# Optimization experiments

Hardware: AMD Instinct MI355X
Metric: run time of the kernel (lower is better)

The kernel has to match this reference:

```python
import jax, jax.numpy as jnp
import numpy as np

NUM_LEVELS = 6
LEVEL_DIM = 4
BASE_RES = 4
HASHMAP_SIZE = 2 ** 19  # torch-ngp default log2_hashmap_size=19
N_SAMPLES = 300
PRIMES = (1, 2654435761, 805459861)
N_RAYS = 16384

# offsets of the 8 trilinear corners, [8,3]
_OFFS = jnp.array([[i, j, k] for i in (0, 1) for j in (0, 1) for k in (0, 1)], dtype=jnp.int32)


def _sample_points_along_ray(starts, ends):
    # starts/ends: [N,2]; lerp 300 points, append ray parameter t as z -> [N,300,3]
    t = jnp.linspace(0.0, 1.0, N_SAMPLES, dtype=starts.dtype)[None, :, None]  # [1,300,1]
    p2 = starts[:, None, :] * (1.0 - t) + ends[:, None, :] * t  # [N,300,2]
    z = jnp.broadcast_to(t, (starts.shape[0], N_SAMPLES, 1))
    return jnp.concatenate([p2, z], axis=-1)


def _grid_encode(points, embeddings):
    # points: [N,S,3] in [0,1]; embeddings: [L, T, D]. Returns [N,S,L*D].
    feats = []
    for l in range(NUM_LEVELS):
        R = BASE_RES * (2 ** l)  # 4,8,16,32,64,128
        pos = points * R
        p0 = jnp.floor(pos).astype(jnp.int32)
        w = pos - p0  # trilinear fractions, [N,S,3]
        corners = jnp.clip(p0[..., None, :] + _OFFS, 0, R)  # [N,S,8,3]
        cw = jnp.where(_OFFS.astype(bool), w[..., None, :], 1.0 - w[..., None, :]).prod(-1)  # [N,S,8]
        if (R + 1) ** 3 <= HASHMAP_SIZE:
            # dense level: row-major vertex index
            idx = corners[..., 0] + corners[..., 1] * (R + 1) + corners[..., 2] * (R + 1) ** 2
        else:
            # hashed level: xor of coord * prime, uint32 wraparound
            c = corners.astype(jnp.uint32)
            idx = ((c[..., 0] * jnp.uint32(PRIMES[0]))
                   ^ (c[..., 1] * jnp.uint32(PRIMES[1]))
                   ^ (c[..., 2] * jnp.uint32(PRIMES[2]))) % jnp.uint32(HASHMAP_SIZE)
            idx = idx.astype(jnp.int32)
        emb = embeddings[l][idx]  # [N,S,8,D] gather
        feats.append((cw[..., None] * emb).sum(-2))  # [N,S,D]
    return jnp.concatenate(feats, axis=-1)  # [N,S,24]


def setup_inputs() -> dict:
    key = jax.random.key(0)
    ks = jax.random.split(key, 12)
    x = jax.random.uniform(ks[0], (N_RAYS, 4), dtype=jnp.float32)
    indices_first = jax.random.randint(ks[1], (N_RAYS,), 0, N_SAMPLES, dtype=jnp.int32)
    # hash-grid tables, torch-ngp init: uniform(-1e-4, 1e-4)
    embeddings = jax.random.uniform(ks[2], (NUM_LEVELS, HASHMAP_SIZE, LEVEL_DIM),
                                    minval=-1e-4, maxval=1e-4, dtype=jnp.float32)
    d_in = NUM_LEVELS * LEVEL_DIM * 5  # 120
    sc = 0.02
    W1 = jax.random.normal(ks[3], (64, d_in), dtype=jnp.float32) * sc
    b1 = jnp.zeros((64,), jnp.float32)
    W2 = jax.random.normal(ks[4], (64, 64), dtype=jnp.float32) * sc
    b2 = jnp.zeros((64,), jnp.float32)
    W3 = jax.random.normal(ks[5], (64, 64), dtype=jnp.float32) * sc
    b3 = jnp.zeros((64,), jnp.float32)
    W4 = jax.random.normal(ks[6], (3, 64), dtype=jnp.float32) * sc
    b4 = jnp.zeros((3,), jnp.float32)
    return {"x": x, "indices_first": indices_first, "embeddings": embeddings,
            "W1": W1, "b1": b1, "W2": W2, "b2": b2, "W3": W3, "b3": b3, "W4": W4, "b4": b4}


def reference(x, indices_first, embeddings, W1, b1, W2, b2, W3, b3, W4, b4):
    pts = jax.lax.stop_gradient(_sample_points_along_ray(x[:, :2], x[:, 2:4]))  # no_grad in original
    pe = _grid_encode(pts, embeddings)  # [N,300,24]
    n = jnp.arange(x.shape[0])
    gather = lambda d: pe[n, jnp.clip(indices_first + d, 0, N_SAMPLES - 1)]
    feat = jnp.concatenate([gather(-2), gather(-1), gather(0), gather(1), gather(2)], axis=-1)  # [N,120]
    h = jax.nn.relu(feat @ W1.T + b1)
    h = jax.nn.relu(h @ W2.T + b2)
    h = jax.nn.relu(h @ W3.T + b3)
    return h @ W4.T + b4  # [N,3]
```

## Files before the change

### kernel.cpp

```cpp
#include <hip/hip_runtime.h>


#define NSAMP 300
#define HSIZE (1u << 19)

__global__ __launch_bounds__(1024, 1) void rgbnet_fused(
    const float4* __restrict__ x,
    const int*    __restrict__ idxf,
    const float4* __restrict__ emb,
    const float* __restrict__ W1, const float* __restrict__ b1,
    const float* __restrict__ W2, const float* __restrict__ b2,
    const float* __restrict__ W3, const float* __restrict__ b3,
    const float* __restrict__ W4, const float* __restrict__ b4,
    float* __restrict__ out, int N)
{
    __shared__ float sFeat[120 * 64];
    __shared__ float sHa[64 * 64];
    __shared__ float sHb[64 * 64];

    const int tid  = threadIdx.x;
    const int r    = tid & 63;
    const int wsub = tid >> 6;
    const int ray  = blockIdx.x * 64 + r;

    {
        const float4 xr = x[ray];
        const int    i0 = idxf[ray];
        const float sx = xr.x, sy = xr.y, ex = xr.z, ey = xr.w;

        for (int p = wsub; p < 30; p += 16) {
            const int d = p / 6;
            const int l = p - d * 6;
            int s = i0 + d - 2;
            s = max(0, min(s, NSAMP - 1));
            const float t   = (float)s * (1.0f / 299.0f);
            const float omt = 1.0f - t;
            const int   R   = 4 << l;
            const float fR  = (float)R;
            const float px = (sx * omt + ex * t) * fR;
            const float py = (sy * omt + ey * t) * fR;
            const float pz = t * fR;
            const float fx0 = floorf(px), fy0 = floorf(py), fz0 = floorf(pz);
            const float wx = px - fx0, wy = py - fy0, wz = pz - fz0;
            const int ix = (int)fx0, iy = (int)fy0, iz = (int)fz0;
            const int Rp1 = R + 1;
            const float4* __restrict__ ebase = emb + (size_t)l * HSIZE;

            float ax = 0.f, ay = 0.f, az = 0.f, aw = 0.f;
            #pragma unroll
            for (int c = 0; c < 8; ++c) {
                const int ox = (c >> 2) & 1, oy = (c >> 1) & 1, oz = c & 1;
                int cx = min(ix + ox, R); cx = max(cx, 0);
                int cy = min(iy + oy, R); cy = max(cy, 0);
                int cz = min(iz + oz, R); cz = max(cz, 0);
                unsigned idx;
                if (l < 5) {
                    idx = (unsigned)(cx + cy * Rp1 + cz * Rp1 * Rp1);
                } else {
                    idx = ((unsigned)cx * 1u
                         ^ (unsigned)cy * 2654435761u
                         ^ (unsigned)cz * 805459861u) & (HSIZE - 1u);
                }
                const float4 e = ebase[idx];
                const float cw = (ox ? wx : 1.f - wx)
                               * (oy ? wy : 1.f - wy)
                               * (oz ? wz : 1.f - wz);
                ax = fmaf(cw, e.x, ax);
                ay = fmaf(cw, e.y, ay);
                az = fmaf(cw, e.z, az);
                aw = fmaf(cw, e.w, aw);
            }
            const int k0 = p * 4;
            sFeat[(k0 + 0) * 64 + r] = ax;
            sFeat[(k0 + 1) * 64 + r] = ay;
            sFeat[(k0 + 2) * 64 + r] = az;
            sFeat[(k0 + 3) * 64 + r] = aw;
        }
    }
    __syncthreads();

    const int wu = __builtin_amdgcn_readfirstlane(wsub);
    const int j0 = wu * 4;

    float hh[4];

    #pragma unroll
    for (int jj = 0; jj < 4; ++jj) hh[jj] = b1[j0 + jj];
    #pragma unroll 8
    for (int k = 0; k < 120; ++k) {
        const float f = sFeat[k * 64 + r];
        #pragma unroll
        for (int jj = 0; jj < 4; ++jj)
            hh[jj] = fmaf(f, W1[(j0 + jj) * 120 + k], hh[jj]);
    }
    #pragma unroll
    for (int jj = 0; jj < 4; ++jj)
        sHa[(j0 + jj) * 64 + r] = fmaxf(hh[jj], 0.f);
    __syncthreads();

    #pragma unroll
    for (int jj = 0; jj < 4; ++jj) hh[jj] = b2[j0 + jj];
    #pragma unroll 8
    for (int k = 0; k < 64; ++k) {
        const float f = sHa[k * 64 + r];
        #pragma unroll
        for (int jj = 0; jj < 4; ++jj)
            hh[jj] = fmaf(f, W2[(j0 + jj) * 64 + k], hh[jj]);
    }
    #pragma unroll
    for (int jj = 0; jj < 4; ++jj)
        sHb[(j0 + jj) * 64 + r] = fmaxf(hh[jj], 0.f);
    __syncthreads();

    #pragma unroll
    for (int jj = 0; jj < 4; ++jj) hh[jj] = b3[j0 + jj];
    #pragma unroll 8
    for (int k = 0; k < 64; ++k) {
        const float f = sHb[k * 64 + r];
        #pragma unroll
        for (int jj = 0; jj < 4; ++jj)
            hh[jj] = fmaf(f, W3[(j0 + jj) * 64 + k], hh[jj]);
    }
    #pragma unroll
    for (int jj = 0; jj < 4; ++jj)
        sHa[(j0 + jj) * 64 + r] = fmaxf(hh[jj], 0.f);
    __syncthreads();

    if (wu < 3) {
        float acc = b4[wu];
        #pragma unroll 8
        for (int k = 0; k < 64; ++k)
            acc = fmaf(sHa[k * 64 + r], W4[wu * 64 + k], acc);
        out[(size_t)ray * 3 + wu] = acc;
    }
}

extern "C" void kernel_launch(void* const* d_in, const int* in_sizes, int n_in,
                              void* d_out, int out_size, void* d_ws, size_t ws_size,
                              hipStream_t stream) {
    const float4* x    = (const float4*)d_in[0];
    const int*    idxf = (const int*)   d_in[1];
    const float4* emb  = (const float4*)d_in[2];
    const float*  W1   = (const float*) d_in[3];
    const float*  b1   = (const float*) d_in[4];
    const float*  W2   = (const float*) d_in[5];
    const float*  b2   = (const float*) d_in[6];
    const float*  W3   = (const float*) d_in[7];
    const float*  b3   = (const float*) d_in[8];
    const float*  W4   = (const float*) d_in[9];
    const float*  b4   = (const float*) d_in[10];
    float* out = (float*)d_out;

    const int N = in_sizes[0] / 4;
    const int blocks = (N + 63) / 64;
    hipLaunchKernelGGL(rgbnet_fused, dim3(blocks), dim3(1024), 0, stream,
                       x, idxf, emb, W1, b1, W2, b2, W3, b3, W4, b4, out, N);
}
```

Baseline: 127.5 us.

## Split fused kernel into high-occupancy encode kernel and separate MLP kernel

Splits the single fused kernel into two launches. The first encodes the hash grid with small 256-thread blocks at high occupancy, one lane per (ray, level, offset) pair, and writes the features to a workspace buffer. The second loads those features into shared memory and runs the MLP as before. The aim is more gather parallelism and better latency hiding for the random embedding loads, at the cost of an extra global round trip for about 8 MB of features and a second launch. It falls back to the fused kernel when the workspace is too small.

Result: no change. 127.8 us (+0.2%).

```diff
diff --git a/kernel.cpp b/kernel.cpp
--- a/kernel.cpp
+++ b/kernel.cpp
@@ -3,6 +3,152 @@
 
 #define NSAMP 300
 #define HSIZE (1u << 19)
+
+__global__ __launch_bounds__(256, 8) void rgbnet_encode(
+    const float4* __restrict__ x,
+    const int*    __restrict__ idxf,
+    const float4* __restrict__ emb,
+    float4*       __restrict__ featG,
+    int N)
+{
+    const int tid  = threadIdx.x;
+    const int lane = tid & 63;
+    const int wv   = tid >> 6;
+    const int rsub = lane >> 5;
+    const int p    = lane & 31;
+    const int ray  = blockIdx.x * 8 + wv * 2 + rsub;
+    if (p >= 30 || ray >= N) return;
+
+    const float4 xr = x[ray];
+    const int d = p / 6;
+    const int l = p - d * 6;
+    int s = idxf[ray] + d - 2;
+    s = max(0, min(s, NSAMP - 1));
+    const float t   = (float)s * (1.0f / 299.0f);
+    const float omt = 1.0f - t;
+    const int   R   = 4 << l;
+    const float fR  = (float)R;
+    const float px = (xr.x * omt + xr.z * t) * fR;
+    const float py = (xr.y * omt + xr.w * t) * fR;
+    const float pz = t * fR;
+    const float fx0 = floorf(px), fy0 = floorf(py), fz0 = floorf(pz);
+    const float wx = px - fx0, wy = py - fy0, wz = pz - fz0;
+    const int ix = (int)fx0, iy = (int)fy0, iz = (int)fz0;
+    const int Rp1 = R + 1;
+    const float4* __restrict__ ebase = emb + (size_t)l * HSIZE;
+
+    float ax = 0.f, ay = 0.f, az = 0.f, aw = 0.f;
+    #pragma unroll
+    for (int c = 0; c < 8; ++c) {
+        const int ox = (c >> 2) & 1, oy = (c >> 1) & 1, oz = c & 1;
+        int cx = min(ix + ox, R); cx = max(cx, 0);
+        int cy = min(iy + oy, R); cy = max(cy, 0);
+        int cz = min(iz + oz, R); cz = max(cz, 0);
+        unsigned idx;
+        if (l < 5) {
+            idx = (unsigned)(cx + cy * Rp1 + cz * Rp1 * Rp1);
+        } else {
+            idx = ((unsigned)cx * 1u
+                 ^ (unsigned)cy * 2654435761u
+                 ^ (unsigned)cz * 805459861u) & (HSIZE - 1u);
+        }
+        const float4 e = ebase[idx];
+        const float cw = (ox ? wx : 1.f - wx)
+                       * (oy ? wy : 1.f - wy)
+                       * (oz ? wz : 1.f - wz);
+        ax = fmaf(cw, e.x, ax);
+        ay = fmaf(cw, e.y, ay);
+        az = fmaf(cw, e.z, az);
+        aw = fmaf(cw, e.w, aw);
+    }
+    featG[(size_t)ray * 30 + p] = make_float4(ax, ay, az, aw);
+}
+
+__global__ __launch_bounds__(1024, 1) void rgbnet_mlp(
+    const float4* __restrict__ featG,
+    const float* __restrict__ W1, const float* __restrict__ b1,
+    const float* __restrict__ W2, const float* __restrict__ b2,
+    const float* __restrict__ W3, const float* __restrict__ b3,
+    const float* __restrict__ W4, const float* __restrict__ b4,
+    float* __restrict__ out, int N)
+{
+    __shared__ float sFeat[120 * 64];
+    __shared__ float sHa[64 * 64];
+    __shared__ float sHb[64 * 64];
+
+    const int tid  = threadIdx.x;
+    const int r    = tid & 63;
+    const int wsub = tid >> 6;
+    const int ray0 = blockIdx.x * 64;
+    const int ray  = ray0 + r;
+
+    for (int j = tid; j < 64 * 30; j += 1024) {
+        const int rr = j / 30;
+        const int k4 = j - rr * 30;
+        const float4 f = featG[(size_t)(ray0 + rr) * 30 + k4];
+        const int k0 = k4 * 4;
+        sFeat[(k0 + 0) * 64 + rr] = f.x;
+        sFeat[(k0 + 1) * 64 + rr] = f.y;
+        sFeat[(k0 + 2) * 64 + rr] = f.z;
+        sFeat[(k0 + 3) * 64 + rr] = f.w;
+    }
+    __syncthreads();
+
+    const int wu = __builtin_amdgcn_readfirstlane(wsub);
+    const int j0 = wu * 4;
+
+    float hh[4];
+
+    #pragma unroll
+    for (int jj = 0; jj < 4; ++jj) hh[jj] = b1[j0 + jj];
+    #pragma unroll 8
+    for (int k = 0; k < 120; ++k) {
+        const float f = sFeat[k * 64 + r];
+        #pragma unroll
+        for (int jj = 0; jj < 4; ++jj)
+            hh[jj] = fmaf(f, W1[(j0 + jj) * 120 + k], hh[jj]);
+    }
+    #pragma unroll
+    for (int jj = 0; jj < 4; ++jj)
+        sHa[(j0 + jj) * 64 + r] = fmaxf(hh[jj], 0.f);
+    __syncthreads();
+
+    #pragma unroll
+    for (int jj = 0; jj < 4; ++jj) hh[jj] = b2[j0 + jj];
+    #pragma unroll 8
+    for (int k = 0; k < 64; ++k) {
+        const float f = sHa[k * 64 + r];
+        #pragma unroll
+        for (int jj = 0; jj < 4; ++jj)
+            hh[jj] = fmaf(f, W2[(j0 + jj) * 64 + k], hh[jj]);
+    }
+    #pragma unroll
+    for (int jj = 0; jj < 4; ++jj)
+        sHb[(j0 + jj) * 64 + r] = fmaxf(hh[jj], 0.f);
+    __syncthreads();
+
+    #pragma unroll
+    for (int jj = 0; jj < 4; ++jj) hh[jj] = b3[j0 + jj];
+    #pragma unroll 8
+    for (int k = 0; k < 64; ++k) {
+        const float f = sHb[k * 64 + r];
+        #pragma unroll
+        for (int jj = 0; jj < 4; ++jj)
+            hh[jj] = fmaf(f, W3[(j0 + jj) * 64 + k], hh[jj]);
+    }
+    #pragma unroll
+    for (int jj = 0; jj < 4; ++jj)
+        sHa[(j0 + jj) * 64 + r] = fmaxf(hh[jj], 0.f);
+    __syncthreads();
+
+    if (wu < 3) {
+        float acc = b4[wu];
+        #pragma unroll 8
+        for (int k = 0; k < 64; ++k)
+            acc = fmaf(sHa[k * 64 + r], W4[wu * 64 + k], acc);
+        out[(size_t)ray * 3 + wu] = acc;
+    }
+}
 
 __global__ __launch_bounds__(1024, 1) void rgbnet_fused(
     const float4* __restrict__ x,
@@ -152,7 +298,16 @@
     float* out = (float*)d_out;
 
     const int N = in_sizes[0] / 4;
-    const int blocks = (N + 63) / 64;
-    hipLaunchKernelGGL(rgbnet_fused, dim3(blocks), dim3(1024), 0, stream,
-                       x, idxf, emb, W1, b1, W2, b2, W3, b3, W4, b4, out, N);
+    const size_t need = (size_t)N * 30 * sizeof(float4);
+
+    if (ws_size >= need) {
+        float4* featG = (float4*)d_ws;
+        hipLaunchKernelGGL(rgbnet_encode, dim3((N + 7) / 8), dim3(256), 0, stream,
+                           x, idxf, emb, featG, N);
+        hipLaunchKernelGGL(rgbnet_mlp, dim3((N + 63) / 64), dim3(1024), 0, stream,
+                           featG, W1, b1, W2, b2, W3, b3, W4, b4, out, N);
+    } else {
+        hipLaunchKernelGGL(rgbnet_fused, dim3((N + 63) / 64), dim3(1024), 0, stream,
+                           x, idxf, emb, W1, b1, W2, b2, W3, b3, W4, b4, out, N);
+    }
 }
```
